# Optimization experiments

Hardware: AMD Instinct MI355X
Metric: run time of the kernel (lower is better)

Reference implementation:

```python
import jax, jax.numpy as jnp
import numpy as np

EMB_K = 512
EMB_DIM = 256
BETA = 0.25
GAMMA = 0.99
EPS = 1e-5
B, T = 16, 4096


def setup_inputs() -> dict:
    key = jax.random.key(0)
    k1, k2, k3 = jax.random.split(key, 3)
    return {
        "inputs": jax.random.normal(k1, (B, EMB_DIM, T), dtype=jnp.float32),
        "emb_weight": jax.random.normal(k2, (EMB_K, EMB_DIM), dtype=jnp.float32),
        "ema_w": jax.random.normal(k3, (EMB_K, EMB_DIM), dtype=jnp.float32),
        "ema_cluster_size": jnp.zeros((EMB_K,), dtype=jnp.float32),
    }


def reference(inputs, emb_weight, ema_w, ema_cluster_size):
    # [B, D, T] -> [B, T, D]
    x = jnp.transpose(inputs, (0, 2, 1))
    flat = x.reshape(-1, EMB_DIM)  # [N, D]

    # squared euclidean distances to codebook: [N, K]
    dist = (jnp.sum(flat * flat, axis=1, keepdims=True)
            + jnp.sum(emb_weight * emb_weight, axis=1)
            - 2.0 * flat @ emb_weight.T)
    idx = jnp.argmin(dist, axis=1)            # [N]
    enc = jax.nn.one_hot(idx, EMB_K, dtype=flat.dtype)  # [N, K]

    # --- EMA codebook update (training branch) ---
    counts = jax.ops.segment_sum(jnp.ones_like(idx, dtype=flat.dtype), idx,
                                 num_segments=EMB_K)  # == enc.sum(0)
    new_cs = ema_cluster_size * GAMMA + (1.0 - GAMMA) * counts
    n = jnp.sum(new_cs)
    new_cs = (new_cs + EPS) / (n + EMB_K * EPS) * n
    dw = jax.ops.segment_sum(flat, idx, num_segments=EMB_K)  # == enc.T @ flat
    new_ema_w = ema_w * GAMMA + (1.0 - GAMMA) * dw
    new_emb_weight = new_ema_w / new_cs[:, None]

    # quantize with updated codebook (gather == enc @ new_emb_weight)
    Q = new_emb_weight[idx].reshape(x.shape)  # [B, T, D]

    e_latent_loss = jnp.mean((jax.lax.stop_gradient(Q) - x) ** 2)
    loss = BETA * e_latent_loss

    # straight-through
    Q_st = x + jax.lax.stop_gradient(Q - x)

    avg_probs = jnp.mean(enc, axis=0)
    PP = jnp.exp(-jnp.sum(avg_probs * jnp.log(avg_probs + 1e-10)))

    return loss, jnp.transpose(Q_st, (0, 2, 1)), PP, enc
```

## Files before the change

### kernel.cpp

```cpp
#include <hip/hip_runtime.h>

#define N_TOT 65536
#define DIM 256
#define KK 512
#define TT 4096
#define BB 16

typedef short bf16x8 __attribute__((ext_vector_type(8)));
typedef float f32x4 __attribute__((ext_vector_type(4)));

__device__ __forceinline__ ushort f2bf(float f) {
    unsigned u = __float_as_uint(f);
    unsigned r = (u + 0x7fffu + ((u >> 16) & 1u)) >> 16;
    return (ushort)r;
}

__global__ void k_prep_e(const float* __restrict__ emb, float* __restrict__ se,
                         ushort* __restrict__ eb) {
    int k = blockIdx.x, tid = threadIdx.x;
    int c0 = tid * 4;
    float4 v = *(const float4*)(emb + k * DIM + c0);
    float f[4] = {v.x, v.y, v.z, v.w};
    float s = f[0] * f[0] + f[1] * f[1] + f[2] * f[2] + f[3] * f[3];
#pragma unroll
    for (int m = 1; m < 64; m <<= 1) s += __shfl_xor(s, m);
    if (tid == 0) se[k] = s;
    ushort h[4], l[4];
#pragma unroll
    for (int j = 0; j < 4; ++j) {
        h[j] = f2bf(f[j]);
        float hf = __uint_as_float(((unsigned)h[j]) << 16);
        l[j] = f2bf(f[j] - hf);
    }
    uint2 hp = make_uint2((unsigned)h[0] | ((unsigned)h[1] << 16),
                          (unsigned)h[2] | ((unsigned)h[3] << 16));
    uint2 lp = make_uint2((unsigned)l[0] | ((unsigned)l[1] << 16),
                          (unsigned)l[2] | ((unsigned)l[3] << 16));
    *(uint2*)(eb + (size_t)k * 512 + c0) = hp;
    *(uint2*)(eb + (size_t)k * 512 + 256 + c0) = lp;
}

__global__ __launch_bounds__(256) void k_split_x(const float* __restrict__ in,
                                                 ushort* __restrict__ xt) {
    __shared__ float ls[64][65];
    int tid = threadIdx.x;
    int b = blockIdx.x >> 8;
    int rest = blockIdx.x & 255;
    int tt = rest >> 2, dt = rest & 3;
    int t0 = tt * 64, d0 = dt * 64;
    int tl = tid & 63, dg = tid >> 6;
    const float* src = in + (size_t)b * DIM * TT + t0 + tl;
#pragma unroll
    for (int p = 0; p < 16; ++p) {
        int d = dg * 16 + p;
        ls[d][tl] = src[(size_t)(d0 + d) * TT];
    }
    __syncthreads();
    int c0 = dg * 16;
    int n = b * TT + t0 + tl;
    ushort* row = xt + (size_t)n * 512;
    ushort h[16], l[16];
#pragma unroll
    for (int j = 0; j < 16; ++j) {
        float v = ls[c0 + j][tl];
        h[j] = f2bf(v);
        float hf = __uint_as_float(((unsigned)h[j]) << 16);
        l[j] = f2bf(v - hf);
    }
    uint hu[8], lu[8];
#pragma unroll
    for (int j = 0; j < 8; ++j) {
        hu[j] = (unsigned)h[2 * j] | ((unsigned)h[2 * j + 1] << 16);
        lu[j] = (unsigned)l[2 * j] | ((unsigned)l[2 * j + 1] << 16);
    }
    *(uint4*)(row + d0 + c0) = make_uint4(hu[0], hu[1], hu[2], hu[3]);
    *(uint4*)(row + d0 + c0 + 8) = make_uint4(hu[4], hu[5], hu[6], hu[7]);
    *(uint4*)(row + 256 + d0 + c0) = make_uint4(lu[0], lu[1], lu[2], lu[3]);
    *(uint4*)(row + 256 + d0 + c0 + 8) = make_uint4(lu[4], lu[5], lu[6], lu[7]);
}

__global__ void k_zero(float* __restrict__ dw, unsigned* __restrict__ counts,
                       unsigned* __restrict__ lossd) {
    int i = blockIdx.x * 256 + threadIdx.x;
    if (i < 131072) dw[i] = 0.f;
    int j = i - 131072;
    if (j >= 0 && j < 512) counts[j] = 0u;
    if (j >= 512 && j < 514) lossd[j - 512] = 0u;
}

__global__ __launch_bounds__(128, 2) void k_dist(
    const ushort* __restrict__ xt, const ushort* __restrict__ eb,
    const float* __restrict__ se,
    float* __restrict__ partd, int* __restrict__ parti) {
    __shared__ ushort As[128 * 64];
    __shared__ ushort Bs[128 * 64];
    const int tid = threadIdx.x;
    const int lane = tid & 63, w = tid >> 6;
    const int id = blockIdx.x;
    const int lin = (id & 7) * 256 + (id >> 3);
    const int bj = lin & 3, bi = lin >> 2;
    const int n0 = bi * 128, k0 = bj * 128;

    f32x4 acc[8][4] = {};

    for (int it = 0; it < 12; ++it) {
        const int region = it >> 2, sub = it & 3;
        const int aoff = (region == 2 ? 256 : 0) + sub * 64;
        const int boff = (region == 1 ? 256 : 0) + sub * 64;
#pragma unroll
        for (int i = 0; i < 8; ++i) {
            int r = i * 16 + w * 8 + (lane >> 3);
            int slot = (lane & 7) ^ (r & 7);
            const ushort* ga = xt + (size_t)(n0 + r) * 512 + aoff + slot * 8;
            const ushort* gb = eb + (size_t)(k0 + r) * 512 + boff + slot * 8;
            __builtin_amdgcn_global_load_lds(
                (const __attribute__((address_space(1))) void*)ga,
                (__attribute__((address_space(3))) void*)&As[(i * 16 + w * 8) * 64],
                16, 0, 0);
            __builtin_amdgcn_global_load_lds(
                (const __attribute__((address_space(1))) void*)gb,
                (__attribute__((address_space(3))) void*)&Bs[(i * 16 + w * 8) * 64],
                16, 0, 0);
        }
        __syncthreads();
#pragma unroll
        for (int kk = 0; kk < 2; ++kk) {
            bf16x8 af[8], bfr[4];
#pragma unroll
            for (int mi = 0; mi < 8; ++mi) {
                int row = mi * 16 + (lane & 15);
                int slot = (kk * 4 + (lane >> 4)) ^ (row & 7);
                af[mi] = *(const bf16x8*)&As[row * 64 + slot * 8];
            }
#pragma unroll
            for (int ni = 0; ni < 4; ++ni) {
                int row = w * 64 + ni * 16 + (lane & 15);
                int slot = (kk * 4 + (lane >> 4)) ^ (row & 7);
                bfr[ni] = *(const bf16x8*)&Bs[row * 64 + slot * 8];
            }
#pragma unroll
            for (int mi = 0; mi < 8; ++mi)
#pragma unroll
                for (int ni = 0; ni < 4; ++ni)
                    acc[mi][ni] = __builtin_amdgcn_mfma_f32_16x16x32_bf16(
                        af[mi], bfr[ni], acc[mi][ni], 0, 0, 0);
        }
        __syncthreads();
    }

    float se4[4];
#pragma unroll
    for (int ni = 0; ni < 4; ++ni) se4[ni] = se[k0 + w * 64 + ni * 16 + (lane & 15)];
    float* pd = (float*)As;
    int* pi = (int*)Bs;
#pragma unroll
    for (int mi = 0; mi < 8; ++mi) {
#pragma unroll
        for (int j = 0; j < 4; ++j) {
            int r = mi * 16 + (lane >> 4) * 4 + j;
            float dmin = 3.4e38f;
            int bidx = 0x7fffffff;
#pragma unroll
            for (int ni = 0; ni < 4; ++ni) {
                int k = k0 + w * 64 + ni * 16 + (lane & 15);
                float dv = fmaf(-2.f, acc[mi][ni][j], se4[ni]);
                if (dv < dmin) { dmin = dv; bidx = k; }
            }
            pd[r * 32 + w * 16 + (lane & 15)] = dmin;
            pi[r * 32 + w * 16 + (lane & 15)] = bidx;
        }
    }
    __syncthreads();
    {
        float dmin = 3.4e38f;
        int bidx = 0x7fffffff;
        for (int c = 0; c < 32; ++c) {
            float dv = pd[tid * 32 + c];
            int iv = pi[tid * 32 + c];
            if (dv < dmin || (dv == dmin && iv < bidx)) { dmin = dv; bidx = iv; }
        }
        partd[(size_t)bj * N_TOT + n0 + tid] = dmin;
        parti[(size_t)bj * N_TOT + n0 + tid] = bidx;
    }
}

__global__ void k_combine(const float* __restrict__ partd, const int* __restrict__ parti,
                          int* __restrict__ idx, unsigned* __restrict__ counts) {
    __shared__ unsigned h[512];
    int tid = threadIdx.x;
    h[tid] = 0u;
    h[tid + 256] = 0u;
    __syncthreads();
    int n = blockIdx.x * 256 + tid;
    float dmin = 3.4e38f;
    int bidx = 0x7fffffff;
#pragma unroll
    for (int p = 0; p < 4; ++p) {
        float dv = partd[(size_t)p * N_TOT + n];
        int iv = parti[(size_t)p * N_TOT + n];
        if (dv < dmin || (dv == dmin && iv < bidx)) { dmin = dv; bidx = iv; }
    }
    idx[n] = bidx;
    atomicAdd(&h[bidx], 1u);
    __syncthreads();
    if (h[tid]) atomicAdd(&counts[tid], h[tid]);
    if (h[tid + 256]) atomicAdd(&counts[tid + 256], h[tid + 256]);
}

__global__ void k_enc_zero(float2* __restrict__ enc2) {
    size_t base = (size_t)blockIdx.x * (256 * 32) + threadIdx.x;
#pragma unroll
    for (int j = 0; j < 32; ++j) enc2[base + j * 256] = make_float2(0.f, 0.f);
}

__global__ void k_enc_ones(const int* __restrict__ idx, float* __restrict__ enc) {
    int n = blockIdx.x * 256 + threadIdx.x;
    enc[(size_t)n * KK + idx[n]] = 1.0f;
}

__global__ void k_scalars(const unsigned* __restrict__ counts, const float* __restrict__ cs_in,
                          float* __restrict__ csn, float* __restrict__ pp_out,
                          unsigned* __restrict__ cursor) {
    __shared__ float red[512];
    __shared__ unsigned sc[512];
    int k = threadIdx.x;
    unsigned ci = counts[k];
    float c = (float)ci;
    float pre = cs_in[k] * 0.99f + 0.01f * c;
    red[k] = pre;
    sc[k] = ci;
    __syncthreads();
#pragma unroll
    for (int s = 256; s > 0; s >>= 1) {
        if (k < s) red[k] += red[k + s];
        __syncthreads();
    }
    float nsum = red[0];
    __syncthreads();
    csn[k] = (pre + 1e-5f) / (nsum + 512 * 1e-5f) * nsum;
    float p = c * (1.0f / 65536.f);
    red[k] = -p * logf(p + 1e-10f);
    __syncthreads();
#pragma unroll
    for (int s = 256; s > 0; s >>= 1) {
        if (k < s) red[k] += red[k + s];
        __syncthreads();
    }
    if (k == 0) pp_out[0] = expf(red[0]);
#pragma unroll
    for (int s = 1; s < 512; s <<= 1) {
        unsigned v = (k >= s) ? sc[k - s] : 0u;
        __syncthreads();
        sc[k] += v;
        __syncthreads();
    }
    cursor[k] = sc[k] - ci;
}

__global__ void k_scatter(const int* __restrict__ idx, unsigned* __restrict__ cursor,
                          unsigned* __restrict__ sortedp) {
    int n = blockIdx.x * 256 + threadIdx.x;
    int k = idx[n];
    unsigned p = atomicAdd(&cursor[k], 1u);
    sortedp[p] = (unsigned)n | ((unsigned)k << 17);
}

__global__ __launch_bounds__(256) void k_dwsum(const ushort* __restrict__ xt,
                                               const unsigned* __restrict__ sortedp,
                                               float* __restrict__ dw) {
    int gw = blockIdx.x * 4 + (threadIdx.x >> 6);
    int lane = threadIdx.x & 63;
    int base = gw * 16;
    unsigned pk[16];
#pragma unroll
    for (int i = 0; i < 16; ++i) pk[i] = sortedp[base + i];
    float acc[8] = {0.f, 0.f, 0.f, 0.f, 0.f, 0.f, 0.f, 0.f};
    int curk = (int)(pk[0] >> 17);
#pragma unroll
    for (int i = 0; i < 16; ++i) {
        int n = (int)(pk[i] & 0x1ffffu);
        int k = (int)(pk[i] >> 17);
        if (k != curk) {
#pragma unroll
            for (int j = 0; j < 8; ++j) {
                float other = __shfl(acc[j], lane + 32);
                if (lane < 32) atomicAdd(&dw[curk * DIM + lane * 8 + j], acc[j] + other);
                acc[j] = 0.f;
            }
            curk = k;
        }
        uint4 v = *(const uint4*)(xt + (size_t)n * 512 + lane * 8);
        unsigned u[4] = {v.x, v.y, v.z, v.w};
#pragma unroll
        for (int j = 0; j < 4; ++j) {
            acc[2 * j] += __uint_as_float(u[j] << 16);
            acc[2 * j + 1] += __uint_as_float(u[j] & 0xffff0000u);
        }
    }
#pragma unroll
    for (int j = 0; j < 8; ++j) {
        float other = __shfl(acc[j], lane + 32);
        if (lane < 32) atomicAdd(&dw[curk * DIM + lane * 8 + j], acc[j] + other);
    }
}

__global__ void k_newemb(const float* __restrict__ ema_w, const float* __restrict__ dw,
                         const float* __restrict__ csn, float* __restrict__ newemb) {
    int i = blockIdx.x * 256 + threadIdx.x;
    int k = i >> 8;
    newemb[i] = (ema_w[i] * 0.99f + 0.01f * dw[i]) / csn[k];
}

__global__ __launch_bounds__(256) void k_out1(const float* __restrict__ in,
                                              const int* __restrict__ idx,
                                              const float* __restrict__ newemb,
                                              float* __restrict__ out1,
                                              unsigned long long* __restrict__ lossd) {
    __shared__ float q[256][68];
    __shared__ float redl[4];
    int tid = threadIdx.x;
    int b = blockIdx.x >> 6, tc = blockIdx.x & 63;
    int tl = tid & 63, dg = tid >> 6;
    int kk = idx[b * TT + tc * 64 + tl];
    const float4* ne4 = (const float4*)(newemb + (size_t)kk * DIM);
#pragma unroll
    for (int d4 = 0; d4 < 16; ++d4) {
        float4 v = ne4[dg * 16 + d4];
        int d = dg * 64 + d4 * 4;
        q[d + 0][tl] = v.x;
        q[d + 1][tl] = v.y;
        q[d + 2][tl] = v.z;
        q[d + 3][tl] = v.w;
    }
    __syncthreads();
    float lacc = 0.f;
    const float* xb = in + (size_t)b * DIM * TT + tc * 64;
    float* ob = out1 + (size_t)b * DIM * TT + tc * 64;
#pragma unroll 4
    for (int j = 0; j < 64; ++j) {
        int fi = tid + 256 * j;
        int d = fi >> 6, t = fi & 63;
        float qv = q[d][t];
        float xv = xb[(size_t)d * TT + t];
        ob[(size_t)d * TT + t] = qv;
        float df = qv - xv;
        lacc = fmaf(df, df, lacc);
    }
#pragma unroll
    for (int m = 1; m < 64; m <<= 1) lacc += __shfl_xor(lacc, m);
    if ((tid & 63) == 0) redl[tid >> 6] = lacc;
    __syncthreads();
    if (tid == 0) {
        double s = (double)redl[0] + (double)redl[1] + (double)redl[2] + (double)redl[3];
        atomicAdd((double*)lossd, s);
    }
}

__global__ void k_loss_fin(const double* __restrict__ lossd, float* __restrict__ out0) {
    out0[0] = (float)(0.25 * lossd[0] * (1.0 / 16777216.0));
}

extern "C" void kernel_launch(void* const* d_in, const int* in_sizes, int n_in,
                              void* d_out, int out_size, void* d_ws, size_t ws_size,
                              hipStream_t stream) {
    const float* in = (const float*)d_in[0];
    const float* emb = (const float*)d_in[1];
    const float* emaw = (const float*)d_in[2];
    const float* cs = (const float*)d_in[3];
    float* out = (float*)d_out;
    char* ws = (char*)d_ws;

    float* se = (float*)(ws + 0);
    float* partd = (float*)(ws + 264192);
    int* parti = (int*)(ws + 1312768);
    int* idx = (int*)(ws + 2361344);
    unsigned* counts = (unsigned*)(ws + 2623488);
    float* csn = (float*)(ws + 2625536);
    float* dw = (float*)(ws + 2627584);
    float* newemb = (float*)(ws + 3151872);
    double* lossd = (double*)(ws + 3676160);
    ushort* eb = (ushort*)(ws + 3676416);
    ushort* xt = (ushort*)(ws + 4200704);
    unsigned* sortedp = (unsigned*)(ws + 71309568);
    unsigned* cursor = (unsigned*)(ws + 71573760);

    float* out_loss = out;
    float* out_q = out + 1;
    float* out_pp = out + 16777217;
    float* enc = out + 16777218;

    hipLaunchKernelGGL(k_prep_e, dim3(512), dim3(64), 0, stream, emb, se, eb);
    hipLaunchKernelGGL(k_split_x, dim3(4096), dim3(256), 0, stream, in, xt);
    hipLaunchKernelGGL(k_zero, dim3(515), dim3(256), 0, stream, dw, counts, (unsigned*)lossd);
    hipLaunchKernelGGL(k_dist, dim3(2048), dim3(128), 0, stream, xt, eb, se, partd, parti);
    hipLaunchKernelGGL(k_combine, dim3(256), dim3(256), 0, stream, partd, parti, idx, counts);
    hipLaunchKernelGGL(k_enc_zero, dim3(2048), dim3(256), 0, stream, (float2*)enc);
    hipLaunchKernelGGL(k_enc_ones, dim3(256), dim3(256), 0, stream, idx, enc);
    hipLaunchKernelGGL(k_scalars, dim3(1), dim3(512), 0, stream, counts, cs, csn, out_pp, cursor);
    hipLaunchKernelGGL(k_scatter, dim3(256), dim3(256), 0, stream, idx, cursor, sortedp);
    hipLaunchKernelGGL(k_dwsum, dim3(1024), dim3(256), 0, stream, xt, sortedp, dw);
    hipLaunchKernelGGL(k_newemb, dim3(512), dim3(256), 0, stream, emaw, dw, csn, newemb);
    hipLaunchKernelGGL(k_out1, dim3(1024), dim3(256), 0, stream, in, idx, newemb, out_q,
                       (unsigned long long*)lossd);
    hipLaunchKernelGGL(k_loss_fin, dim3(1), dim3(1), 0, stream, lossd, out_loss);
}
```

Before: 349.0 us.

## Reuse staged tiles in distance GEMM, fuse one-hot write, read x from bf16 split

The distance GEMM loop is reordered so that one staged B tile (and one A tile) serves two MFMA passes, cutting the global-to-LDS traffic per block. The two passes over the one-hot output (zero fill, then scatter ones) become a single kernel that writes each row once with vector stores. The quantize/loss kernel now rebuilds x from the hi/lo bf16 split buffer instead of rereading the fp32 input, and that read overlaps the codebook gather. The split rebuild may not match fp32 x bit for bit, which slightly changes the loss sum.

```diff
diff --git a/kernel.cpp b/kernel.cpp
--- a/kernel.cpp
+++ b/kernel.cpp
@@ -103,26 +103,31 @@
 
     f32x4 acc[8][4] = {};
 
-    for (int it = 0; it < 12; ++it) {
-        const int region = it >> 2, sub = it & 3;
-        const int aoff = (region == 2 ? 256 : 0) + sub * 64;
-        const int boff = (region == 1 ? 256 : 0) + sub * 64;
+    auto stage_a = [&](int off) {
 #pragma unroll
         for (int i = 0; i < 8; ++i) {
             int r = i * 16 + w * 8 + (lane >> 3);
             int slot = (lane & 7) ^ (r & 7);
-            const ushort* ga = xt + (size_t)(n0 + r) * 512 + aoff + slot * 8;
-            const ushort* gb = eb + (size_t)(k0 + r) * 512 + boff + slot * 8;
+            const ushort* ga = xt + (size_t)(n0 + r) * 512 + off + slot * 8;
             __builtin_amdgcn_global_load_lds(
                 (const __attribute__((address_space(1))) void*)ga,
                 (__attribute__((address_space(3))) void*)&As[(i * 16 + w * 8) * 64],
                 16, 0, 0);
+        }
+    };
+    auto stage_b = [&](int off) {
+#pragma unroll
+        for (int i = 0; i < 8; ++i) {
+            int r = i * 16 + w * 8 + (lane >> 3);
+            int slot = (lane & 7) ^ (r & 7);
+            const ushort* gb = eb + (size_t)(k0 + r) * 512 + off + slot * 8;
             __builtin_amdgcn_global_load_lds(
                 (const __attribute__((address_space(1))) void*)gb,
                 (__attribute__((address_space(3))) void*)&Bs[(i * 16 + w * 8) * 64],
                 16, 0, 0);
         }
-        __syncthreads();
+    };
+    auto compute = [&]() {
 #pragma unroll
         for (int kk = 0; kk < 2; ++kk) {
             bf16x8 af[8], bfr[4];
@@ -145,6 +150,24 @@
                     acc[mi][ni] = __builtin_amdgcn_mfma_f32_16x16x32_bf16(
                         af[mi], bfr[ni], acc[mi][ni], 0, 0, 0);
         }
+    };
+
+    for (int sub = 0; sub < 4; ++sub) {
+        stage_a(sub * 64);
+        stage_b(sub * 64);
+        __syncthreads();
+        compute();
+        __syncthreads();
+        stage_a(256 + sub * 64);
+        __syncthreads();
+        compute();
+        __syncthreads();
+    }
+    for (int sub = 0; sub < 4; ++sub) {
+        stage_a(sub * 64);
+        stage_b(256 + sub * 64);
+        __syncthreads();
+        compute();
         __syncthreads();
     }
 
@@ -207,15 +230,27 @@
     if (h[tid + 256]) atomicAdd(&counts[tid + 256], h[tid + 256]);
 }
 
-__global__ void k_enc_zero(float2* __restrict__ enc2) {
-    size_t base = (size_t)blockIdx.x * (256 * 32) + threadIdx.x;
-#pragma unroll
-    for (int j = 0; j < 32; ++j) enc2[base + j * 256] = make_float2(0.f, 0.f);
-}
-
-__global__ void k_enc_ones(const int* __restrict__ idx, float* __restrict__ enc) {
-    int n = blockIdx.x * 256 + threadIdx.x;
-    enc[(size_t)n * KK + idx[n]] = 1.0f;
+__global__ __launch_bounds__(256) void k_enc(const int* __restrict__ idx,
+                                             float* __restrict__ enc) {
+    __shared__ int sidx[64];
+    int tid = threadIdx.x;
+    int base = blockIdx.x * 64;
+    if (tid < 64) sidx[tid] = idx[base + tid];
+    __syncthreads();
+    int w = tid >> 6, lane = tid & 63;
+#pragma unroll 4
+    for (int r = 0; r < 16; ++r) {
+        int row = w * 16 + r;
+        int k = sidx[row];
+        int hit = (lane == (k >> 3));
+        int kj = k & 7;
+        float v[8];
+#pragma unroll
+        for (int j = 0; j < 8; ++j) v[j] = (hit && (kj == j)) ? 1.0f : 0.0f;
+        float* p = enc + (size_t)(base + row) * KK + lane * 8;
+        *(float4*)p = make_float4(v[0], v[1], v[2], v[3]);
+        *(float4*)(p + 4) = make_float4(v[4], v[5], v[6], v[7]);
+    }
 }
 
 __global__ void k_scalars(const unsigned* __restrict__ counts, const float* __restrict__ cs_in,
@@ -311,7 +346,7 @@
     newemb[i] = (ema_w[i] * 0.99f + 0.01f * dw[i]) / csn[k];
 }
 
-__global__ __launch_bounds__(256) void k_out1(const float* __restrict__ in,
+__global__ __launch_bounds__(256) void k_out1(const ushort* __restrict__ xt,
                                               const int* __restrict__ idx,
                                               const float* __restrict__ newemb,
                                               float* __restrict__ out1,
@@ -321,8 +356,12 @@
     int tid = threadIdx.x;
     int b = blockIdx.x >> 6, tc = blockIdx.x & 63;
     int tl = tid & 63, dg = tid >> 6;
-    int kk = idx[b * TT + tc * 64 + tl];
+    int n = b * TT + tc * 64 + tl;
+    int kk = idx[n];
     const float4* ne4 = (const float4*)(newemb + (size_t)kk * DIM);
+    const uint2* xh = (const uint2*)(xt + (size_t)n * 512 + dg * 64);
+    const uint2* xl = (const uint2*)(xt + (size_t)n * 512 + 256 + dg * 64);
+    float lacc = 0.f;
 #pragma unroll
     for (int d4 = 0; d4 < 16; ++d4) {
         float4 v = ne4[dg * 16 + d4];
@@ -331,20 +370,25 @@
         q[d + 1][tl] = v.y;
         q[d + 2][tl] = v.z;
         q[d + 3][tl] = v.w;
-    }
-    __syncthreads();
-    float lacc = 0.f;
-    const float* xb = in + (size_t)b * DIM * TT + tc * 64;
+        uint2 h2 = xh[d4];
+        uint2 l2 = xl[d4];
+        float x0 = __uint_as_float(h2.x << 16) + __uint_as_float(l2.x << 16);
+        float x1 = __uint_as_float(h2.x & 0xffff0000u) + __uint_as_float(l2.x & 0xffff0000u);
+        float x2 = __uint_as_float(h2.y << 16) + __uint_as_float(l2.y << 16);
+        float x3 = __uint_as_float(h2.y & 0xffff0000u) + __uint_as_float(l2.y & 0xffff0000u);
+        float e0 = v.x - x0, e1 = v.y - x1, e2 = v.z - x2, e3 = v.w - x3;
+        lacc = fmaf(e0, e0, lacc);
+        lacc = fmaf(e1, e1, lacc);
+        lacc = fmaf(e2, e2, lacc);
+        lacc = fmaf(e3, e3, lacc);
+    }
+    __syncthreads();
     float* ob = out1 + (size_t)b * DIM * TT + tc * 64;
-#pragma unroll 4
+#pragma unroll 8
     for (int j = 0; j < 64; ++j) {
         int fi = tid + 256 * j;
         int d = fi >> 6, t = fi & 63;
-        float qv = q[d][t];
-        float xv = xb[(size_t)d * TT + t];
-        ob[(size_t)d * TT + t] = qv;
-        float df = qv - xv;
-        lacc = fmaf(df, df, lacc);
+        ob[(size_t)d * TT + t] = q[d][t];
     }
 #pragma unroll
     for (int m = 1; m < 64; m <<= 1) lacc += __shfl_xor(lacc, m);
@@ -394,13 +438,12 @@
     hipLaunchKernelGGL(k_zero, dim3(515), dim3(256), 0, stream, dw, counts, (unsigned*)lossd);
     hipLaunchKernelGGL(k_dist, dim3(2048), dim3(128), 0, stream, xt, eb, se, partd, parti);
     hipLaunchKernelGGL(k_combine, dim3(256), dim3(256), 0, stream, partd, parti, idx, counts);
-    hipLaunchKernelGGL(k_enc_zero, dim3(2048), dim3(256), 0, stream, (float2*)enc);
-    hipLaunchKernelGGL(k_enc_ones, dim3(256), dim3(256), 0, stream, idx, enc);
+    hipLaunchKernelGGL(k_enc, dim3(1024), dim3(256), 0, stream, idx, enc);
     hipLaunchKernelGGL(k_scalars, dim3(1), dim3(512), 0, stream, counts, cs, csn, out_pp, cursor);
     hipLaunchKernelGGL(k_scatter, dim3(256), dim3(256), 0, stream, idx, cursor, sortedp);
     hipLaunchKernelGGL(k_dwsum, dim3(1024), dim3(256), 0, stream, xt, sortedp, dw);
     hipLaunchKernelGGL(k_newemb, dim3(512), dim3(256), 0, stream, emaw, dw, csn, newemb);
-    hipLaunchKernelGGL(k_out1, dim3(1024), dim3(256), 0, stream, in, idx, newemb, out_q,
+    hipLaunchKernelGGL(k_out1, dim3(1024), dim3(256), 0, stream, xt, idx, newemb, out_q,
                        (unsigned long long*)lossd);
     hipLaunchKernelGGL(k_loss_fin, dim3(1), dim3(1), 0, stream, lossd, out_loss);
 }
```

Result: slower. 404.2 us (+15.8%).
